# Kernel optimization log

Measured on AMD Instinct MI355X. Metric: run time of the kernel, lower is better.

Reference implementation:

```python
import jax, jax.numpy as jnp
import numpy as np

WEIGHTS = (0.5, 1.0, 2.0)   # per-channel weights (init kwarg)
INVERTED = True             # init kwarg


def setup_inputs() -> dict:
    key = jax.random.key(0)
    B, C, H, W = 16, 3, 256, 256
    # binary flood mask: nonzero = foreground (scipy EDT measures distance to nearest zero)
    flood = jax.random.randint(key, (B, C, H, W), 0, 2).astype(jnp.float32)
    return {"flood_batch": flood}


def _edt_squared(mask):
    """Exact squared Euclidean distance transform per [H,W] slice.

    mask: bool [B,C,H,W], True = foreground (nonzero). Returns float32 [B,C,H,W]
    squared distance from each True pixel to the nearest False pixel (0 at False).
    Uses the exact separable decomposition:
      D2[r,w] = min_{r'} ( g[r',w]^2 + (r-r')^2 ),  g = 1D horizontal distance to zero.
    """
    B, C, H, W = mask.shape
    BIG = jnp.float32(H + W)  # exceeds any achievable 1D distance

    # --- pass 1: 1D distance to nearest zero along W (forward + backward scans) ---
    m = jnp.moveaxis(mask, -1, 0)  # [W,B,C,H]

    def step(carry, mm):
        d = jnp.where(mm, jnp.minimum(carry + 1.0, BIG), 0.0)
        return d, d

    init = jnp.full((B, C, H), BIG, jnp.float32)
    _, fwd = jax.lax.scan(step, init, m)
    _, bwd = jax.lax.scan(step, init, m[::-1])
    g = jnp.minimum(fwd, bwd[::-1])          # [W,B,C,H]
    g2 = jnp.moveaxis(g, 0, -1) ** 2          # [B,C,H,W]

    # --- pass 2: exact min-plus over rows (vectorized over B,C,W; scan over output row) ---
    rows = jnp.arange(H, dtype=jnp.float32)

    def row_step(_, r):
        cand = g2 + ((r - rows) ** 2)[None, None, :, None]  # [B,C,H,W]
        return None, cand.min(axis=2)                        # [B,C,W]

    _, d2 = jax.lax.scan(row_step, None, rows)  # [H,B,C,W]
    return jnp.moveaxis(d2, 0, 2)               # [B,C,H,W]


def reference(flood_batch):
    w = jnp.asarray(WEIGHTS, jnp.float32)
    dt = jnp.sqrt(_edt_squared(flood_batch != 0))            # [B,C,H,W]
    dt = dt * w[None, :, None, None]                         # per-channel weight
    mx = dt.max(axis=(2, 3), keepdims=True)                  # per-slice max
    safe = jnp.where(mx > 0, mx, 1.0)
    scaled = (mx - dt) / safe if INVERTED else dt / safe
    return jnp.where(mx > 0, scaled, dt)
```

## Files before the change

kernel.cpp:

```cpp
#include <hip/hip_runtime.h>


#define BIGD 512.0f

__global__ __launch_bounds__(256) void k1_rowpass(const float* __restrict__ in,
                                                  float* __restrict__ g2out) {
    int row = blockIdx.x * 4 + (threadIdx.x >> 6);
    int lane = threadIdx.x & 63;
    const float4 m = ((const float4*)in)[(long)row * 64 + lane];

    unsigned long long bz[4];
    bz[0] = __ballot(m.x == 0.f);
    bz[1] = __ballot(m.y == 0.f);
    bz[2] = __ballot(m.z == 0.f);
    bz[3] = __ballot(m.w == 0.f);

    auto nz2 = [&](int p) -> float {
        int dist = 512;
        #pragma unroll
        for (int cc = 0; cc < 4; ++cc) {
            unsigned long long M = bz[cc];
            int q = p - cc;
            int qa = (q < 0) ? 0 : q;
            int tp = qa >> 2;
            unsigned long long Ml = (q >= 0) ? (M & (~0ull >> (63 - tp))) : 0ull;
            int tn = (q < 0) ? 0 : ((q + 3) >> 2);
            unsigned long long Mh = (tn < 64) ? (M & (~0ull << tn)) : 0ull;
            if (Ml) dist = min(dist, q - 4 * (63 - __builtin_clzll(Ml)));
            if (Mh) dist = min(dist, 4 * __builtin_ctzll(Mh) - q);
        }
        float fd = (float)dist;
        return fd * fd;
    };

    int p0 = 4 * lane;
    float4 g;
    g.x = nz2(p0 + 0);
    g.y = nz2(p0 + 1);
    g.z = nz2(p0 + 2);
    g.w = nz2(p0 + 3);
    ((float4*)g2out)[(long)row * 64 + lane] = g;
}

#define PADV 1e30f
__global__ __launch_bounds__(256) void k2_colpass(const float* __restrict__ g2,
                                                  float* __restrict__ d2out,
                                                  float* __restrict__ stripmax) {
    __shared__ float tile[16 * 289];
    __shared__ float wm[4];
    int bx = blockIdx.x;
    int slice = bx >> 4;
    int w0 = (bx & 15) * 16;
    int tid = threadIdx.x;
    const float* src = g2 + (long)slice * 65536 + w0;

    {
        int c = tid >> 4, i = tid & 15;
        tile[c * 289 + i] = PADV;
        tile[c * 289 + 272 + i] = PADV;
    }
    #pragma unroll
    for (int it = 0; it < 4; ++it) {
        int f = it * 256 + tid;
        int row = f >> 2;
        int quad = f & 3;
        float4 v = *((const float4*)(src + (long)row * 256) + quad);
        int cb = quad * 4;
        tile[(cb + 0) * 289 + 16 + row] = v.x;
        tile[(cb + 1) * 289 + 16 + row] = v.y;
        tile[(cb + 2) * 289 + 16 + row] = v.z;
        tile[(cb + 3) * 289 + 16 + row] = v.w;
    }
    __syncthreads();

    int c = tid & 15;
    int r0 = (tid >> 4) * 16;

    float s[48];
    #pragma unroll
    for (int i = 0; i < 48; ++i) s[i] = tile[c * 289 + r0 + i];

    float dmin[16];
    #pragma unroll
    for (int k = 0; k < 16; ++k) dmin[k] = s[k + 16];
    #pragma unroll
    for (int o = -16; o <= 16; ++o) {
        if (o == 0) continue;
        float oo = (float)(o * o);
        #pragma unroll
        for (int k = 0; k < 16; ++k)
            dmin[k] = fminf(dmin[k], s[k + 16 + o] + oo);
    }

    float* dst = d2out + (long)slice * 65536 + w0 + c;
    float m = 0.f;
    #pragma unroll
    for (int k = 0; k < 16; ++k) {
        dst[(long)(r0 + k) * 256] = dmin[k];
        m = fmaxf(m, dmin[k]);
    }

    #pragma unroll
    for (int off = 32; off >= 1; off >>= 1)
        m = fmaxf(m, __shfl_down(m, off, 64));
    if ((tid & 63) == 0) wm[tid >> 6] = m;
    __syncthreads();
    if (tid == 0)
        stripmax[bx] = fmaxf(fmaxf(wm[0], wm[1]), fmaxf(wm[2], wm[3]));
}

__global__ __launch_bounds__(256) void k2_fix(const float* __restrict__ in,
                                              float* __restrict__ d2,
                                              float* __restrict__ stripmax) {
    int slice = blockIdx.x;
    int t = threadIdx.x;
    __shared__ float sm;
    if (t < 16) {
        float v = stripmax[slice * 16 + t];
        #pragma unroll
        for (int off = 8; off >= 1; off >>= 1) v = fmaxf(v, __shfl_down(v, off, 64));
        if (t == 0) sm = v;
    }
    __syncthreads();
    if (sm <= 288.0f) return;

    {
        const float* rin = in + (long)slice * 65536 + (long)t * 256;
        float* rout = d2 + (long)slice * 65536 + (long)t * 256;
        float f[256];
        float carry = BIGD;
        for (int i = 0; i < 256; ++i) {
            carry = (rin[i] != 0.f) ? fminf(carry + 1.f, BIGD) : 0.f;
            f[i] = carry;
        }
        carry = BIGD;
        for (int i = 255; i >= 0; --i) {
            carry = (rin[i] != 0.f) ? fminf(carry + 1.f, BIGD) : 0.f;
            float g = fminf(f[i], carry);
            rout[i] = g * g;
        }
    }
    __threadfence();
    __syncthreads();

    float col[256];
    float* base = d2 + (long)slice * 65536 + t;
    for (int r = 0; r < 256; ++r) col[r] = base[(long)r * 256];
    float mx = 0.f;
    for (int r = 0; r < 256; ++r) {
        float best = 3e38f;
        for (int rp = 0; rp < 256; ++rp) {
            float dr = (float)(r - rp);
            best = fminf(best, fmaf(dr, dr, col[rp]));
        }
        base[(long)r * 256] = best;
        mx = fmaxf(mx, best);
    }
    __shared__ float red[4];
    #pragma unroll
    for (int off = 32; off >= 1; off >>= 1) mx = fmaxf(mx, __shfl_down(mx, off, 64));
    if ((t & 63) == 0) red[t >> 6] = mx;
    __syncthreads();
    if (t == 0) {
        float m = fmaxf(fmaxf(red[0], red[1]), fmaxf(red[2], red[3]));
        #pragma unroll
        for (int i = 0; i < 16; ++i) stripmax[slice * 16 + i] = m;
    }
}

__global__ __launch_bounds__(256) void k3_final(float* __restrict__ out,
                                                const float* __restrict__ stripmax) {
    __shared__ float sMx;
    int tid = threadIdx.x;
    int idx4 = blockIdx.x * 256 + tid;
    int slice = blockIdx.x >> 6;
    if (tid < 16) {
        float v = stripmax[slice * 16 + tid];
        #pragma unroll
        for (int off = 8; off >= 1; off >>= 1) v = fmaxf(v, __shfl_down(v, off, 64));
        if (tid == 0) sMx = v;
    }
    __syncthreads();

    int c = slice % 3;
    float wgt = (c == 0) ? 0.5f : ((c == 1) ? 1.0f : 2.0f);
    float mx = wgt * __builtin_sqrtf(sMx);

    float4 d2 = ((float4*)out)[idx4];
    float4 r;
    if (mx > 0.f) {
        float inv = 1.0f / mx;
        r.x = (mx - wgt * __builtin_sqrtf(d2.x)) * inv;
        r.y = (mx - wgt * __builtin_sqrtf(d2.y)) * inv;
        r.z = (mx - wgt * __builtin_sqrtf(d2.z)) * inv;
        r.w = (mx - wgt * __builtin_sqrtf(d2.w)) * inv;
    } else {
        r.x = wgt * __builtin_sqrtf(d2.x);
        r.y = wgt * __builtin_sqrtf(d2.y);
        r.z = wgt * __builtin_sqrtf(d2.z);
        r.w = wgt * __builtin_sqrtf(d2.w);
    }
    ((float4*)out)[idx4] = r;
}

extern "C" void kernel_launch(void* const* d_in, const int* in_sizes, int n_in,
                              void* d_out, int out_size, void* d_ws, size_t ws_size,
                              hipStream_t stream) {
    const float* in = (const float*)d_in[0];
    float* out = (float*)d_out;
    float* stripmax = (float*)d_ws;

    k1_rowpass<<<3072, 256, 0, stream>>>(in, out);
    k2_colpass<<<768, 256, 0, stream>>>(out, out, stripmax);
    k2_fix<<<48, 256, 0, stream>>>(in, out, stripmax);
    k3_final<<<3072, 256, 0, stream>>>(out, stripmax);
}
```

Before: 87.49 us.

## Compress rows to zero-bitmasks and compute row distances inside column pass

The first kernel now writes only per-row ballot bitmasks (32 bytes per row) instead of a full float g² image. The column-pass kernel loads the slice bitmask into shared memory and computes the horizontal squared distances itself, which removes a full float write and read of the intermediate. The separate fix-up kernel is replaced by a per-pixel fallback to a full 256-row scan when the windowed result exceeds the window bound. This trades global traffic and one launch for redundant bitmask decoding and possible divergence in the fallback loop.

Result: faster. 83.01 us (-5.1%).

```diff
diff --git a/kernel.cpp b/kernel.cpp
--- a/kernel.cpp
+++ b/kernel.cpp
@@ -2,24 +2,57 @@
 
 
 #define BIGD 512.0f
+#define PADV 1e30f
 
-__global__ __launch_bounds__(256) void k1_rowpass(const float* __restrict__ in,
-                                                  float* __restrict__ g2out) {
+__global__ __launch_bounds__(256) void k1_bitmask(const float* __restrict__ in,
+                                                  unsigned long long* __restrict__ bits) {
     int row = blockIdx.x * 4 + (threadIdx.x >> 6);
     int lane = threadIdx.x & 63;
     const float4 m = ((const float4*)in)[(long)row * 64 + lane];
 
-    unsigned long long bz[4];
-    bz[0] = __ballot(m.x == 0.f);
-    bz[1] = __ballot(m.y == 0.f);
-    bz[2] = __ballot(m.z == 0.f);
-    bz[3] = __ballot(m.w == 0.f);
+    unsigned long long b0 = __ballot(m.x == 0.f);
+    unsigned long long b1 = __ballot(m.y == 0.f);
+    unsigned long long b2 = __ballot(m.z == 0.f);
+    unsigned long long b3 = __ballot(m.w == 0.f);
+    if (lane == 0) {
+        ulonglong4* dst = (ulonglong4*)(bits + (long)row * 4);
+        ulonglong4 v; v.x = b0; v.y = b1; v.z = b2; v.w = b3;
+        *dst = v;
+    }
+}
 
-    auto nz2 = [&](int p) -> float {
+__global__ __launch_bounds__(256) void k2_colpass(const unsigned long long* __restrict__ bits,
+                                                  float* __restrict__ d2out,
+                                                  float* __restrict__ stripmax) {
+    __shared__ unsigned long long bm[1024];
+    __shared__ float tile[16 * 289];
+    __shared__ float wm[4];
+    int bx = blockIdx.x;
+    int slice = bx >> 4;
+    int w0 = (bx & 15) * 16;
+    int tid = threadIdx.x;
+
+    {
+        const unsigned long long* src = bits + (long)slice * 1024;
+        #pragma unroll
+        for (int i = 0; i < 4; ++i) bm[i * 256 + tid] = src[i * 256 + tid];
+    }
+    {
+        int c = tid >> 4, i = tid & 15;
+        tile[c * 289 + i] = PADV;
+        tile[c * 289 + 272 + i] = PADV;
+    }
+    __syncthreads();
+
+    int c = tid & 15;
+    int p = w0 + c;
+    int rg = tid >> 4;
+
+    auto nz2 = [&](int row) -> float {
         int dist = 512;
         #pragma unroll
         for (int cc = 0; cc < 4; ++cc) {
-            unsigned long long M = bz[cc];
+            unsigned long long M = bm[row * 4 + cc];
             int q = p - cc;
             int qa = (q < 0) ? 0 : q;
             int tp = qa >> 2;
@@ -33,49 +66,14 @@
         return fd * fd;
     };
 
-    int p0 = 4 * lane;
-    float4 g;
-    g.x = nz2(p0 + 0);
-    g.y = nz2(p0 + 1);
-    g.z = nz2(p0 + 2);
-    g.w = nz2(p0 + 3);
-    ((float4*)g2out)[(long)row * 64 + lane] = g;
-}
-
-#define PADV 1e30f
-__global__ __launch_bounds__(256) void k2_colpass(const float* __restrict__ g2,
-                                                  float* __restrict__ d2out,
-                                                  float* __restrict__ stripmax) {
-    __shared__ float tile[16 * 289];
-    __shared__ float wm[4];
-    int bx = blockIdx.x;
-    int slice = bx >> 4;
-    int w0 = (bx & 15) * 16;
-    int tid = threadIdx.x;
-    const float* src = g2 + (long)slice * 65536 + w0;
-
-    {
-        int c = tid >> 4, i = tid & 15;
-        tile[c * 289 + i] = PADV;
-        tile[c * 289 + 272 + i] = PADV;
-    }
     #pragma unroll
-    for (int it = 0; it < 4; ++it) {
-        int f = it * 256 + tid;
-        int row = f >> 2;
-        int quad = f & 3;
-        float4 v = *((const float4*)(src + (long)row * 256) + quad);
-        int cb = quad * 4;
-        tile[(cb + 0) * 289 + 16 + row] = v.x;
-        tile[(cb + 1) * 289 + 16 + row] = v.y;
-        tile[(cb + 2) * 289 + 16 + row] = v.z;
-        tile[(cb + 3) * 289 + 16 + row] = v.w;
+    for (int k = 0; k < 16; ++k) {
+        int r = rg + 16 * k;
+        tile[c * 289 + 16 + r] = nz2(r);
     }
     __syncthreads();
 
-    int c = tid & 15;
-    int r0 = (tid >> 4) * 16;
-
+    int r0 = rg * 16;
     float s[48];
     #pragma unroll
     for (int i = 0; i < 48; ++i) s[i] = tile[c * 289 + r0 + i];
@@ -92,6 +90,19 @@
             dmin[k] = fminf(dmin[k], s[k + 16 + o] + oo);
     }
 
+    #pragma unroll
+    for (int k = 0; k < 16; ++k) {
+        if (dmin[k] > 288.0f) {
+            float best = dmin[k];
+            int r = r0 + k;
+            for (int rp = 0; rp < 256; ++rp) {
+                float dr = (float)(r - rp);
+                best = fminf(best, fmaf(dr, dr, tile[c * 289 + 16 + rp]));
+            }
+            dmin[k] = best;
+        }
+    }
+
     float* dst = d2out + (long)slice * 65536 + w0 + c;
     float m = 0.f;
     #pragma unroll
@@ -99,7 +110,6 @@
         dst[(long)(r0 + k) * 256] = dmin[k];
         m = fmaxf(m, dmin[k]);
     }
-
     #pragma unroll
     for (int off = 32; off >= 1; off >>= 1)
         m = fmaxf(m, __shfl_down(m, off, 64));
@@ -107,65 +117,6 @@
     __syncthreads();
     if (tid == 0)
         stripmax[bx] = fmaxf(fmaxf(wm[0], wm[1]), fmaxf(wm[2], wm[3]));
-}
-
-__global__ __launch_bounds__(256) void k2_fix(const float* __restrict__ in,
-                                              float* __restrict__ d2,
-                                              float* __restrict__ stripmax) {
-    int slice = blockIdx.x;
-    int t = threadIdx.x;
-    __shared__ float sm;
-    if (t < 16) {
-        float v = stripmax[slice * 16 + t];
-        #pragma unroll
-        for (int off = 8; off >= 1; off >>= 1) v = fmaxf(v, __shfl_down(v, off, 64));
-        if (t == 0) sm = v;
-    }
-    __syncthreads();
-    if (sm <= 288.0f) return;
-
-    {
-        const float* rin = in + (long)slice * 65536 + (long)t * 256;
-        float* rout = d2 + (long)slice * 65536 + (long)t * 256;
-        float f[256];
-        float carry = BIGD;
-        for (int i = 0; i < 256; ++i) {
-            carry = (rin[i] != 0.f) ? fminf(carry + 1.f, BIGD) : 0.f;
-            f[i] = carry;
-        }
-        carry = BIGD;
-        for (int i = 255; i >= 0; --i) {
-            carry = (rin[i] != 0.f) ? fminf(carry + 1.f, BIGD) : 0.f;
-            float g = fminf(f[i], carry);
-            rout[i] = g * g;
-        }
-    }
-    __threadfence();
-    __syncthreads();
-
-    float col[256];
-    float* base = d2 + (long)slice * 65536 + t;
-    for (int r = 0; r < 256; ++r) col[r] = base[(long)r * 256];
-    float mx = 0.f;
-    for (int r = 0; r < 256; ++r) {
-        float best = 3e38f;
-        for (int rp = 0; rp < 256; ++rp) {
-            float dr = (float)(r - rp);
-            best = fminf(best, fmaf(dr, dr, col[rp]));
-        }
-        base[(long)r * 256] = best;
-        mx = fmaxf(mx, best);
-    }
-    __shared__ float red[4];
-    #pragma unroll
-    for (int off = 32; off >= 1; off >>= 1) mx = fmaxf(mx, __shfl_down(mx, off, 64));
-    if ((t & 63) == 0) red[t >> 6] = mx;
-    __syncthreads();
-    if (t == 0) {
-        float m = fmaxf(fmaxf(red[0], red[1]), fmaxf(red[2], red[3]));
-        #pragma unroll
-        for (int i = 0; i < 16; ++i) stripmax[slice * 16 + i] = m;
-    }
 }
 
 __global__ __launch_bounds__(256) void k3_final(float* __restrict__ out,
@@ -209,9 +160,9 @@
     const float* in = (const float*)d_in[0];
     float* out = (float*)d_out;
     float* stripmax = (float*)d_ws;
+    unsigned long long* bits = (unsigned long long*)((char*)d_ws + 4096);
 
-    k1_rowpass<<<3072, 256, 0, stream>>>(in, out);
-    k2_colpass<<<768, 256, 0, stream>>>(out, out, stripmax);
-    k2_fix<<<48, 256, 0, stream>>>(in, out, stripmax);
+    k1_bitmask<<<3072, 256, 0, stream>>>(in, bits);
+    k2_colpass<<<768, 256, 0, stream>>>(bits, out, stripmax);
     k3_final<<<3072, 256, 0, stream>>>(out, stripmax);
 }
```
